# Optimization experiments

Measured on AMD Instinct MI355X. Metric: run time of the kernel, lower is better.

## Reference

```python
import jax, jax.numpy as jnp
import numpy as np

NEG_SLOPE = 0.2  # PyG GATConv default negative_slope
NUM_GRAPHS = 64


def gat_conv(x, src, dst, W, a_src, a_dst, bias, concat):
    """PyG-style GATConv (eval mode, self-loops already appended to src/dst)."""
    N = x.shape[0]
    H, C = a_src.shape
    h = (x @ W).reshape(N, H, C)                      # [N,H,C]
    al_s = jnp.sum(h * a_src, axis=-1)                # [N,H]
    al_d = jnp.sum(h * a_dst, axis=-1)                # [N,H]
    e = jax.nn.leaky_relu(al_s[src] + al_d[dst], NEG_SLOPE)  # [E,H]
    # numerically-stable segment softmax over incoming edges of each dst node
    m = jax.ops.segment_max(e, dst, num_segments=N)   # [N,H]
    ex = jnp.exp(e - m[dst])
    denom = jax.ops.segment_sum(ex, dst, num_segments=N)
    alpha = ex / (denom[dst] + 1e-16)                 # [E,H]
    out = jax.ops.segment_sum(h[src] * alpha[:, :, None], dst, num_segments=N)  # [N,H,C]
    out = out.reshape(N, H * C) if concat else out.mean(axis=1)
    return out + bias


def setup_inputs() -> dict:
    key = jax.random.key(0)
    ks = jax.random.split(key, 32)
    N, E, F_in, H = 20000, 100000, 128, 8
    x = jax.random.normal(ks[0], (N, F_in), jnp.float32)
    edge_index = jax.random.randint(ks[1], (2, E), 0, N, dtype=jnp.int32)
    batch = jnp.sort(jax.random.randint(ks[2], (N,), 0, NUM_GRAPHS, dtype=jnp.int32))
    inp = {"x": x, "edge_index": edge_index, "batch": batch}
    # (fan_in, per-head channels) for conv1..conv_final
    dims = [(F_in, 64), (512, 256), (2048, 256), (2048, 256), (2048, 256)]
    ki = 3
    for i, (fi, c) in enumerate(dims, 1):
        concat = i < 5
        inp[f"W{i}"] = jax.random.normal(ks[ki], (fi, H * c), jnp.float32) * (1.0 / np.sqrt(fi)); ki += 1
        inp[f"a_src{i}"] = jax.random.normal(ks[ki], (H, c), jnp.float32) * 0.1; ki += 1
        inp[f"a_dst{i}"] = jax.random.normal(ks[ki], (H, c), jnp.float32) * 0.1; ki += 1
        inp[f"b{i}"] = jnp.zeros((H * c if concat else c,), jnp.float32)
    inp["W_lin"] = jax.random.normal(ks[ki], (256, 128), jnp.float32) * (1.0 / np.sqrt(256))
    inp["b_lin"] = jnp.zeros((128,), jnp.float32)
    return inp


def reference(x, edge_index, batch,
              W1, a_src1, a_dst1, b1,
              W2, a_src2, a_dst2, b2,
              W3, a_src3, a_dst3, b3,
              W4, a_src4, a_dst4, b4,
              W5, a_src5, a_dst5, b5,
              W_lin, b_lin):
    N = x.shape[0]
    loop = jnp.arange(N, dtype=edge_index.dtype)  # GATConv add_self_loops=True
    src = jnp.concatenate([edge_index[0], loop])
    dst = jnp.concatenate([edge_index[1], loop])
    h = jax.nn.elu(gat_conv(x, src, dst, W1, a_src1, a_dst1, b1, True))
    h = jax.nn.elu(gat_conv(h, src, dst, W2, a_src2, a_dst2, b2, True))
    h = jax.nn.elu(gat_conv(h, src, dst, W3, a_src3, a_dst3, b3, True))
    h = jax.nn.elu(gat_conv(h, src, dst, W4, a_src4, a_dst4, b4, True))
    h = jax.nn.elu(gat_conv(h, src, dst, W5, a_src5, a_dst5, b5, False))
    sums = jax.ops.segment_sum(h, batch, num_segments=NUM_GRAPHS)
    counts = jax.ops.segment_sum(jnp.ones((N, 1), h.dtype), batch, num_segments=NUM_GRAPHS)
    pooled = jax.nn.elu(sums / jnp.maximum(counts, 1.0))  # global_mean_pool + elu
    return pooled @ W_lin + b_lin
```

## Files before the change

### kernel.cpp

```cpp
#include <hip/hip_runtime.h>
#include <hip/hip_fp16.h>
#include <math.h>

#define NHEADS 8
#define NG 64

typedef _Float16 half8_t __attribute__((ext_vector_type(8)));
typedef _Float16 half4_t __attribute__((ext_vector_type(4)));
typedef float    float4_t __attribute__((ext_vector_type(4)));
typedef __attribute__((address_space(1))) const void g_void;
typedef __attribute__((address_space(3))) void l_void;

__device__ __forceinline__ float elu_f(float x)   { return x > 0.f ? x : expf(x) - 1.f; }
__device__ __forceinline__ float lrelu_f(float x) { return x >= 0.f ? x : 0.2f * x; }

__device__ __forceinline__ float4 ld4(const float* p) { return *(const float4*)p; }
__device__ __forceinline__ float4 ld4(const __half* p) {
    const __half2* q = (const __half2*)p;
    __half2 a = q[0], b = q[1];
    return make_float4(__half2float(a.x), __half2float(a.y),
                       __half2float(b.x), __half2float(b.y));
}
__device__ __forceinline__ void st4(float* p, float4 v) { *(float4*)p = v; }
__device__ __forceinline__ void st4(__half* p, float4 v) {
    __half2 a, b;
    a.x = __float2half(v.x); a.y = __float2half(v.y);
    b.x = __float2half(v.z); b.y = __float2half(v.w);
    __half2* q = (__half2*)p; q[0] = a; q[1] = b;
}
__device__ __forceinline__ float scl(float v)  { return v; }
__device__ __forceinline__ float scl(__half v) { return __half2float(v); }
__device__ __forceinline__ void sst(float* p, float v)  { *p = v; }
__device__ __forceinline__ void sst(__half* p, float v) { *p = __float2half(v); }

struct h4s { __half a, b, c, d; };

__global__ void hist_kernel(const int* __restrict__ ei, int E, int Etot, int* __restrict__ counts) {
    int e = blockIdx.x * blockDim.x + threadIdx.x;
    if (e >= Etot) return;
    int dst = (e < E) ? ei[E + e] : (e - E);
    atomicAdd(&counts[dst], 1);
}

__global__ __launch_bounds__(256) void scan_kernel(const int* __restrict__ counts,
                                                   int* __restrict__ offsets,
                                                   int* __restrict__ cursor, int N) {
    __shared__ int wsum[4];
    const int tid = threadIdx.x;
    const int lane = tid & 63, wid = tid >> 6;
    int carry = 0;
    for (int base = 0; base < N; base += 1024) {
        int i0 = base + tid * 4;
        int v0 = 0, v1 = 0, v2 = 0, v3 = 0;
        if (i0 + 3 < N) {
            int4 q = *(const int4*)(counts + i0);
            v0 = q.x; v1 = q.y; v2 = q.z; v3 = q.w;
        } else {
            if (i0     < N) v0 = counts[i0];
            if (i0 + 1 < N) v1 = counts[i0 + 1];
            if (i0 + 2 < N) v2 = counts[i0 + 2];
            if (i0 + 3 < N) v3 = counts[i0 + 3];
        }
        int tsum = v0 + v1 + v2 + v3;
        int incl = tsum;
#pragma unroll
        for (int off = 1; off < 64; off <<= 1) {
            int t = __shfl_up(incl, off);
            if (lane >= off) incl += t;
        }
        if (lane == 63) wsum[wid] = incl;
        __syncthreads();
        int woff = carry;
        for (int w = 0; w < wid; ++w) woff += wsum[w];
        int o0 = woff + incl - tsum;
        int o1 = o0 + v0, o2 = o1 + v1, o3 = o2 + v2;
        if (i0     < N) { offsets[i0]     = o0; cursor[i0]     = o0; }
        if (i0 + 1 < N) { offsets[i0 + 1] = o1; cursor[i0 + 1] = o1; }
        if (i0 + 2 < N) { offsets[i0 + 2] = o2; cursor[i0 + 2] = o2; }
        if (i0 + 3 < N) { offsets[i0 + 3] = o3; cursor[i0 + 3] = o3; }
        __syncthreads();
        carry += wsum[0] + wsum[1] + wsum[2] + wsum[3];
    }
    if (tid == 0) offsets[N] = carry;
}

__global__ void scatter_kernel(const int* __restrict__ ei, int E, int Etot,
                               int* __restrict__ cursor, int* __restrict__ perm_src) {
    int e = blockIdx.x * blockDim.x + threadIdx.x;
    if (e >= Etot) return;
    int src, dst;
    if (e < E) { src = ei[e]; dst = ei[E + e]; }
    else       { src = e - E; dst = e - E; }
    int pos = atomicAdd(&cursor[dst], 1);
    perm_src[pos] = src;
}

struct PrepArgs {
    const float* x; __half* x16; long n4;
    const float* W[5]; __half* T[5];
    int K[5], Nn[5];
    int b0;
    int tb[5];
};

__global__ __launch_bounds__(256) void prep_kernel(PrepArgs a) {
    int bid = blockIdx.x;
    if (bid < a.b0) {
        long i = (long)bid * 256 + threadIdx.x;
        if (i < a.n4) {
            float4 v = ((const float4*)a.x)[i];
            h4s o; o.a = __float2half(v.x); o.b = __float2half(v.y);
            o.c = __float2half(v.z); o.d = __float2half(v.w);
            ((h4s*)a.x16)[i] = o;
        }
        return;
    }
    int l = 0, base = a.b0;
#pragma unroll
    for (int j = 0; j < 4; ++j) if (bid >= a.tb[j]) { l = j + 1; base = a.tb[j]; }
    const float* W = a.W[l]; __half* T = a.T[l];
    int K = a.K[l], Nn = a.Nn[l];
    int t = bid - base;
    int tilesx = Nn >> 5;
    int nb = (t % tilesx) * 32, kb = (t / tilesx) * 32;
    __shared__ float tt[32][33];
    int tx = threadIdx.x & 31, ty = threadIdx.x >> 5;
#pragma unroll
    for (int r = 0; r < 32; r += 8)
        tt[ty + r][tx] = W[(size_t)(kb + ty + r) * Nn + nb + tx];
    __syncthreads();
#pragma unroll
    for (int r = 0; r < 32; r += 8)
        T[(size_t)(nb + ty + r) * K + kb + tx] = __float2half(tt[tx][ty + r]);
}

__global__ __launch_bounds__(256) void gemm_mfma_kernel(const __half* __restrict__ A,
                                                        const __half* __restrict__ Bt,
                                                        __half* __restrict__ C,
                                                        int M, int N, int K) {
    __shared__ __align__(16) __half Asm[128 * 64];
    __shared__ __align__(16) __half Bsm[128 * 64];
    const int tid  = threadIdx.x;
    const int lane = tid & 63;
    const int wave = tid >> 6;

    const int nwg = (int)(gridDim.x * gridDim.y);
    const int lin = (int)(blockIdx.y * gridDim.x + blockIdx.x);
    const int q = nwg >> 3, r = nwg & 7;
    const int xcd = lin & 7, idx = lin >> 3;
    const int nid = (xcd < r ? xcd * (q + 1) : r * (q + 1) + (xcd - r) * q) + idx;
    const int bx = nid % (int)gridDim.x;
    const int by = nid / (int)gridDim.x;
    const int row0 = by * 128;
    const int col0 = bx * 128;

    const int l15 = lane & 15;
    const int l4  = lane >> 4;
    const int wm  = (wave >> 1) * 64;
    const int wn  = (wave & 1) * 64;

    const int sl_row = lane >> 3;
    const int sl_kch = (lane & 7) ^ sl_row;

    float4_t acc[4][4];
#pragma unroll
    for (int i = 0; i < 4; ++i)
#pragma unroll
        for (int j = 0; j < 4; ++j)
            acc[i][j] = (float4_t){0.f, 0.f, 0.f, 0.f};

    for (int k0 = 0; k0 < K; k0 += 64) {
#pragma unroll
        for (int i = 0; i < 4; ++i) {
            int rr = (i * 4 + wave) * 8 + sl_row;
            int ar = row0 + rr; if (ar >= M) ar = M - 1;
            const __half* ga = A + (size_t)ar * K + k0 + sl_kch * 8;
            char* la = (char*)Asm + ((i * 4 + wave) * 1024 + lane * 16);
            __builtin_amdgcn_global_load_lds((g_void*)ga, (l_void*)la, 16, 0, 0);
            const __half* gb = Bt + (size_t)(col0 + rr) * K + k0 + sl_kch * 8;
            char* lb = (char*)Bsm + ((i * 4 + wave) * 1024 + lane * 16);
            __builtin_amdgcn_global_load_lds((g_void*)gb, (l_void*)lb, 16, 0, 0);
        }
        __syncthreads();
#pragma unroll
        for (int kh = 0; kh < 2; ++kh) {
            half8_t af[4], bf[4];
#pragma unroll
            for (int f = 0; f < 4; ++f) {
                int rowa = wm + f * 16 + l15;
                int ca = (kh * 4 + l4) ^ (rowa & 7);
                af[f] = *(const half8_t*)((const char*)Asm + rowa * 128 + ca * 16);
                int rowb = wn + f * 16 + l15;
                int cb = (kh * 4 + l4) ^ (rowb & 7);
                bf[f] = *(const half8_t*)((const char*)Bsm + rowb * 128 + cb * 16);
            }
#pragma unroll
            for (int fm = 0; fm < 4; ++fm)
#pragma unroll
                for (int fn = 0; fn < 4; ++fn)
                    acc[fm][fn] = __builtin_amdgcn_mfma_f32_16x16x32_f16(af[fm], bf[fn], acc[fm][fn], 0, 0, 0);
        }
        __syncthreads();
    }

#pragma unroll
    for (int fm = 0; fm < 4; ++fm) {
#pragma unroll
        for (int r2 = 0; r2 < 4; ++r2) {
            int row = row0 + wm + fm * 16 + l4 * 4 + r2;
            if (row < M) {
#pragma unroll
                for (int fn = 0; fn < 4; ++fn) {
                    int col = col0 + wn + fn * 16 + l15;
                    C[(size_t)row * N + col] = __float2half(acc[fm][fn][r2]);
                }
            }
        }
    }
}

template <typename TA, typename TC>
__global__ __launch_bounds__(256) void gemm_kernel(const TA* __restrict__ A,
                                                   const float* __restrict__ B,
                                                   TC* __restrict__ C,
                                                   int M, int N, int K) {
    __shared__ float As[16][64];
    __shared__ float Bs[16][64];
    const int tid  = threadIdx.x;
    const int row0 = blockIdx.y * 64, col0 = blockIdx.x * 64;
    const int am = tid >> 2, ak = (tid & 3) << 2;
    const int bk = tid >> 4, bn = (tid & 15) << 2;
    const int ty = (tid >> 4) << 2, tx = (tid & 15) << 2;
    float acc[4][4] = {};
    const int arow = row0 + am;
    for (int k0 = 0; k0 < K; k0 += 16) {
        float4 a4 = make_float4(0.f, 0.f, 0.f, 0.f);
        if (arow < M) a4 = ld4(A + (size_t)arow * K + k0 + ak);
        As[ak + 0][am] = a4.x; As[ak + 1][am] = a4.y;
        As[ak + 2][am] = a4.z; As[ak + 3][am] = a4.w;
        *(float4*)&Bs[bk][bn] = *(const float4*)(B + (size_t)(k0 + bk) * N + col0 + bn);
        __syncthreads();
#pragma unroll
        for (int k = 0; k < 16; ++k) {
            float4 ar = *(const float4*)&As[k][ty];
            float4 br = *(const float4*)&Bs[k][tx];
            acc[0][0] += ar.x * br.x; acc[0][1] += ar.x * br.y; acc[0][2] += ar.x * br.z; acc[0][3] += ar.x * br.w;
            acc[1][0] += ar.y * br.x; acc[1][1] += ar.y * br.y; acc[1][2] += ar.y * br.z; acc[1][3] += ar.y * br.w;
            acc[2][0] += ar.z * br.x; acc[2][1] += ar.z * br.y; acc[2][2] += ar.z * br.z; acc[2][3] += ar.z * br.w;
            acc[3][0] += ar.w * br.x; acc[3][1] += ar.w * br.y; acc[3][2] += ar.w * br.z; acc[3][3] += ar.w * br.w;
        }
        __syncthreads();
    }
#pragma unroll
    for (int i = 0; i < 4; ++i) {
        int r = row0 + ty + i;
        if (r < M) {
            float4 o = make_float4(acc[i][0], acc[i][1], acc[i][2], acc[i][3]);
            st4(C + (size_t)r * N + col0 + tx, o);
        }
    }
}

template <int C>
__global__ void al_vec_kernel(const __half* __restrict__ ht, const float* __restrict__ a_src,
                              const float* __restrict__ a_dst, float* __restrict__ al_s,
                              float* __restrict__ al_d, int N) {
    int wid  = (int)((blockIdx.x * blockDim.x + threadIdx.x) >> 6);
    int lane = threadIdx.x & 63;
    if (wid >= N * NHEADS) return;
    int n = wid / NHEADS, h = wid % NHEADS;
    float ss = 0.f, sd = 0.f;
    int c0 = lane * 4;
    if (c0 < C) {
        const __half* hp = ht + (size_t)n * (NHEADS * C) + h * C + c0;
        half4_t v = *(const half4_t*)hp;
        float4 as4 = *(const float4*)(a_src + h * C + c0);
        float4 ad4 = *(const float4*)(a_dst + h * C + c0);
        float v0 = (float)v[0], v1 = (float)v[1], v2 = (float)v[2], v3 = (float)v[3];
        ss = v0 * as4.x + v1 * as4.y + v2 * as4.z + v3 * as4.w;
        sd = v0 * ad4.x + v1 * ad4.y + v2 * ad4.z + v3 * ad4.w;
    }
#pragma unroll
    for (int off = 32; off > 0; off >>= 1) {
        ss += __shfl_down(ss, off);
        sd += __shfl_down(sd, off);
    }
    if (lane == 0) { al_s[wid] = ss; al_d[wid] = sd; }
}

template <int HC, int C, int MODE>
__global__ __launch_bounds__(256) void agg_fused_kernel(const __half* __restrict__ ht,
                                                        const float* __restrict__ al_s,
                                                        const float* __restrict__ al_d,
                                                        const int* __restrict__ offsets,
                                                        const int* __restrict__ perm_src,
                                                        const float* __restrict__ bias,
                                                        void* __restrict__ outv, int N) {
    constexpr int V = HC / 256;
    int n = blockIdx.x;
    int tid = threadIdx.x;
    int lane = tid & 63;
    const int head = (tid * V) / C;
    int s = offsets[n], e = offsets[n + 1];

    int h2 = lane & 7, es = lane >> 3;
    float ad2 = al_d[(size_t)n * 8 + h2];
    float m = -1e30f;
    for (int p0 = s + es; p0 < e; p0 += 8)
        m = fmaxf(m, lrelu_f(al_s[(size_t)perm_src[p0] * 8 + h2] + ad2));
#pragma unroll
    for (int off = 8; off < 64; off <<= 1) m = fmaxf(m, __shfl_xor(m, off));
    float den = 0.f;
    for (int p0 = s + es; p0 < e; p0 += 8)
        den += expf(lrelu_f(al_s[(size_t)perm_src[p0] * 8 + h2] + ad2) - m);
#pragma unroll
    for (int off = 8; off < 64; off <<= 1) den += __shfl_xor(den, off);
    float inv0 = 1.f / (den + 1e-16f);
    float mh   = __shfl(m, head);
    float invh = __shfl(inv0, head);
    float adh  = __shfl(ad2, head);

    float acc[V];
#pragma unroll
    for (int i = 0; i < V; ++i) acc[i] = 0.f;
    const __half* base = ht + (size_t)tid * V;
    int p = s;
    for (; p + 4 <= e; p += 4) {
        int s0 = perm_src[p], s1 = perm_src[p + 1], s2 = perm_src[p + 2], s3 = perm_src[p + 3];
        float a0 = expf(lrelu_f(al_s[(size_t)s0 * 8 + head] + adh) - mh);
        float a1 = expf(lrelu_f(al_s[(size_t)s1 * 8 + head] + adh) - mh);
        float a2 = expf(lrelu_f(al_s[(size_t)s2 * 8 + head] + adh) - mh);
        float a3 = expf(lrelu_f(al_s[(size_t)s3 * 8 + head] + adh) - mh);
        if (V == 8) {
            half8_t v0 = *(const half8_t*)(base + (size_t)s0 * HC);
            half8_t v1 = *(const half8_t*)(base + (size_t)s1 * HC);
            half8_t v2 = *(const half8_t*)(base + (size_t)s2 * HC);
            half8_t v3 = *(const half8_t*)(base + (size_t)s3 * HC);
#pragma unroll
            for (int i = 0; i < 8; ++i) acc[i] += a0 * (float)v0[i];
#pragma unroll
            for (int i = 0; i < 8; ++i) acc[i] += a1 * (float)v1[i];
#pragma unroll
            for (int i = 0; i < 8; ++i) acc[i] += a2 * (float)v2[i];
#pragma unroll
            for (int i = 0; i < 8; ++i) acc[i] += a3 * (float)v3[i];
        } else {
            __half2 w0 = *(const __half2*)(base + (size_t)s0 * HC);
            __half2 w1 = *(const __half2*)(base + (size_t)s1 * HC);
            __half2 w2 = *(const __half2*)(base + (size_t)s2 * HC);
            __half2 w3 = *(const __half2*)(base + (size_t)s3 * HC);
            acc[0] += a0 * __half2float(w0.x); acc[1] += a0 * __half2float(w0.y);
            acc[0] += a1 * __half2float(w1.x); acc[1] += a1 * __half2float(w1.y);
            acc[0] += a2 * __half2float(w2.x); acc[1] += a2 * __half2float(w2.y);
            acc[0] += a3 * __half2float(w3.x); acc[1] += a3 * __half2float(w3.y);
        }
    }
    for (; p < e; ++p) {
        int src = perm_src[p];
        float a = expf(lrelu_f(al_s[(size_t)src * 8 + head] + adh) - mh);
        const __half* hp = base + (size_t)src * HC;
        if (V == 8) {
            half8_t v = *(const half8_t*)hp;
#pragma unroll
            for (int i = 0; i < 8; ++i) acc[i] += a * (float)v[i];
        } else {
            __half2 v2 = *(const __half2*)hp;
            acc[0] += a * __half2float(v2.x);
            acc[1] += a * __half2float(v2.y);
        }
    }
    if (MODE == 0) {
        __half* out = (__half*)outv;
        if (V == 8) {
            half8_t o;
#pragma unroll
            for (int i = 0; i < 8; ++i)
                o[i] = (_Float16)elu_f(acc[i] * invh + bias[tid * 8 + i]);
            *(half8_t*)(out + (size_t)n * HC + tid * 8) = o;
        } else {
            __half2 o;
            o.x = __float2half(elu_f(acc[0] * invh + bias[tid * 2 + 0]));
            o.y = __float2half(elu_f(acc[1] * invh + bias[tid * 2 + 1]));
            *(__half2*)(out + (size_t)n * HC + tid * 2) = o;
        }
    } else {
        __shared__ float sm[256][8];
#pragma unroll
        for (int i = 0; i < 8; ++i) sm[tid][i] = acc[i] * invh;
        __syncthreads();
        float ssum = 0.f;
#pragma unroll
        for (int h = 0; h < 8; ++h) ssum += sm[h * 32 + (tid >> 3)][tid & 7];
        float* out = (float*)outv;
        out[(size_t)n * C + tid] = elu_f(ssum * (1.f / NHEADS) + bias[tid]);
    }
}

template <typename TH>
__global__ void al_kernel(const TH* __restrict__ ht, const float* __restrict__ a_src,
                          const float* __restrict__ a_dst, float* __restrict__ al_s,
                          float* __restrict__ al_d, int N, int C) {
    int wid  = (int)((blockIdx.x * blockDim.x + threadIdx.x) >> 6);
    int lane = threadIdx.x & 63;
    if (wid >= N * NHEADS) return;
    int n = wid / NHEADS, h = wid % NHEADS;
    const TH* hp = ht + (size_t)n * (NHEADS * C) + h * C;
    float ss = 0.f, sd = 0.f;
    for (int c = lane; c < C; c += 64) {
        float v = scl(hp[c]);
        ss += v * a_src[h * C + c];
        sd += v * a_dst[h * C + c];
    }
#pragma unroll
    for (int off = 32; off > 0; off >>= 1) {
        ss += __shfl_down(ss, off);
        sd += __shfl_down(sd, off);
    }
    if (lane == 0) { al_s[wid] = ss; al_d[wid] = sd; }
}

__global__ void alpha_kernel(const int* __restrict__ offsets, const int* __restrict__ perm_src,
                             const float* __restrict__ al_s, const float* __restrict__ al_d,
                             float* __restrict__ alpha, int N) {
    int idx = blockIdx.x * blockDim.x + threadIdx.x;
    if (idx >= N * NHEADS) return;
    int n = idx / NHEADS, h = idx % NHEADS;
    int s = offsets[n], e = offsets[n + 1];
    float ad = al_d[idx];
    float m = -1e30f;
    for (int p = s; p < e; ++p) {
        float v = lrelu_f(al_s[perm_src[p] * NHEADS + h] + ad);
        m = fmaxf(m, v);
    }
    float denom = 0.f;
    for (int p = s; p < e; ++p) {
        float v  = lrelu_f(al_s[perm_src[p] * NHEADS + h] + ad);
        float ex = expf(v - m);
        alpha[(size_t)p * NHEADS + h] = ex;
        denom += ex;
    }
    float inv = 1.f / (denom + 1e-16f);
    for (int p = s; p < e; ++p) alpha[(size_t)p * NHEADS + h] *= inv;
}

template <int HC, int C, int MODE, typename TH, typename TO>
__global__ __launch_bounds__(256) void agg_kernel(const TH* __restrict__ ht,
                                                  const float* __restrict__ alpha,
                                                  const int* __restrict__ offsets,
                                                  const int* __restrict__ perm_src,
                                                  const float* __restrict__ bias,
                                                  TO* __restrict__ out, int N) {
    constexpr int PER = HC / 256;
    int n = blockIdx.x;
    int tid = threadIdx.x;
    float acc[PER];
#pragma unroll
    for (int i = 0; i < PER; ++i) acc[i] = 0.f;
    int s = offsets[n], e = offsets[n + 1];
    for (int p = s; p < e; ++p) {
        int src = perm_src[p];
        const TH* hp = ht + (size_t)src * HC;
#pragma unroll
        for (int i = 0; i < PER; ++i) {
            int j = tid + i * 256;
            float a = alpha[(size_t)p * NHEADS + (j / C)];
            acc[i] += a * scl(hp[j]);
        }
    }
    if (MODE == 0) {
#pragma unroll
        for (int i = 0; i < PER; ++i) {
            int j = tid + i * 256;
            sst(&out[(size_t)n * HC + j], elu_f(acc[i] + bias[j]));
        }
    } else {
        float srow = 0.f;
#pragma unroll
        for (int i = 0; i < PER; ++i) srow += acc[i];
        sst(&out[(size_t)n * C + tid], elu_f(srow * (1.f / NHEADS) + bias[tid]));
    }
}

__global__ void gstart_kernel(const int* __restrict__ batch, int* __restrict__ gstart, int N) {
    int n = blockIdx.x * blockDim.x + threadIdx.x;
    if (n > N) return;
    if (n == 0) {
        int b0 = batch[0];
        for (int g = 0; g <= b0; ++g) gstart[g] = 0;
    } else if (n == N) {
        int bl = batch[N - 1];
        for (int g = bl + 1; g <= NG; ++g) gstart[g] = N;
    } else {
        int bp = batch[n - 1], bc = batch[n];
        for (int g = bp + 1; g <= bc; ++g) gstart[g] = n;
    }
}

__global__ void pool_kernel(const float* __restrict__ h5, const int* __restrict__ gstart,
                            float* __restrict__ pooled) {
    int g = blockIdx.x, c = threadIdx.x;
    int s = gstart[g], e = gstart[g + 1];
    float sum = 0.f;
    for (int n = s; n < e; ++n) sum += h5[(size_t)n * 256 + c];
    float cnt = fmaxf((float)(e - s), 1.f);
    pooled[g * 256 + c] = elu_f(sum / cnt);
}

__global__ void linear_kernel(const float* __restrict__ pooled, const float* __restrict__ W,
                              const float* __restrict__ b, float* __restrict__ out) {
    int g = blockIdx.x, c = threadIdx.x;
    float s = b[c];
    for (int k = 0; k < 256; ++k) s += pooled[g * 256 + k] * W[k * 128 + c];
    out[g * 128 + c] = s;
}

__device__ __forceinline__ int lb_dev(const int* a, int n, int key) {
    int lo = 0, hi = n;
    while (lo < hi) { int mid = (lo + hi) >> 1; if (a[mid] < key) lo = mid + 1; else hi = mid; }
    return lo;
}

__global__ __launch_bounds__(256) void pool_linear_kernel(const float* __restrict__ h5,
                                                          const int* __restrict__ batch, int N,
                                                          const float* __restrict__ Wlin,
                                                          const float* __restrict__ blin,
                                                          float* __restrict__ out) {
    int g = blockIdx.x, c = threadIdx.x;
    int s = lb_dev(batch, N, g);
    int e = lb_dev(batch, N, g + 1);
    __shared__ float pooled_s[256];
    float sum = 0.f;
    for (int n = s; n < e; ++n) sum += h5[(size_t)n * 256 + c];
    float cnt = fmaxf((float)(e - s), 1.f);
    pooled_s[c] = elu_f(sum / cnt);
    __syncthreads();
    if (c < 128) {
        float acc = blin[c];
        for (int k = 0; k < 256; ++k) acc += pooled_s[k] * Wlin[k * 128 + c];
        out[g * 128 + c] = acc;
    }
}

template <typename TIO, typename TH>
static void run_pipeline(const float* x, const float* const* W, const float* const* asrc,
                         const float* const* adst, const float* const* bias,
                         char* rawIO, char* rawHT,
                         float* al_s, float* al_d, float* alpha_buf,
                         const int* offsets, const int* perm_src,
                         int N, hipStream_t stream) {
    TIO* bufIO = (TIO*)rawIO;
    TH*  bufHT = (TH*)rawHT;
    {
        dim3 g(512 / 64, (N + 63) / 64);
        gemm_kernel<float, TH><<<g, 256, 0, stream>>>(x, W[0], bufHT, N, 512, 128);
        al_kernel<TH><<<(N * NHEADS * 64 + 255) / 256, 256, 0, stream>>>(bufHT, asrc[0], adst[0], al_s, al_d, N, 64);
        alpha_kernel<<<(N * NHEADS + 255) / 256, 256, 0, stream>>>(offsets, perm_src, al_s, al_d, alpha_buf, N);
        agg_kernel<512, 64, 0, TH, TIO><<<N, 256, 0, stream>>>(bufHT, alpha_buf, offsets, perm_src, bias[0], bufIO, N);
    }
    int Kdim = 512;
    for (int l = 1; l < 5; ++l) {
        dim3 g(2048 / 64, (N + 63) / 64);
        gemm_kernel<TIO, TH><<<g, 256, 0, stream>>>(bufIO, W[l], bufHT, N, 2048, Kdim);
        al_kernel<TH><<<(N * NHEADS * 64 + 255) / 256, 256, 0, stream>>>(bufHT, asrc[l], adst[l], al_s, al_d, N, 256);
        alpha_kernel<<<(N * NHEADS + 255) / 256, 256, 0, stream>>>(offsets, perm_src, al_s, al_d, alpha_buf, N);
        if (l < 4)
            agg_kernel<2048, 256, 0, TH, TIO><<<N, 256, 0, stream>>>(bufHT, alpha_buf, offsets, perm_src, bias[l], bufIO, N);
        else
            agg_kernel<2048, 256, 1, TH, float><<<N, 256, 0, stream>>>(bufHT, alpha_buf, offsets, perm_src, bias[l], (float*)rawIO, N);
        Kdim = 2048;
    }
}

extern "C" void kernel_launch(void* const* d_in, const int* in_sizes, int n_in,
                              void* d_out, int out_size, void* d_ws, size_t ws_size,
                              hipStream_t stream) {
    const float* x     = (const float*)d_in[0];
    const int*   ei    = (const int*)d_in[1];
    const int*   batch = (const int*)d_in[2];
    const float* W[5]    = {(const float*)d_in[3],  (const float*)d_in[7],  (const float*)d_in[11],
                            (const float*)d_in[15], (const float*)d_in[19]};
    const float* asrc[5] = {(const float*)d_in[4],  (const float*)d_in[8],  (const float*)d_in[12],
                            (const float*)d_in[16], (const float*)d_in[20]};
    const float* adst[5] = {(const float*)d_in[5],  (const float*)d_in[9],  (const float*)d_in[13],
                            (const float*)d_in[17], (const float*)d_in[21]};
    const float* bias[5] = {(const float*)d_in[6],  (const float*)d_in[10], (const float*)d_in[14],
                            (const float*)d_in[18], (const float*)d_in[22]};
    const float* Wlin = (const float*)d_in[23];
    const float* blin = (const float*)d_in[24];

    const int N    = in_sizes[0] / 128;
    const int E    = in_sizes[1] / 2;
    const int Etot = E + N;

    auto align256 = [](size_t b) { return (b + 255) & ~(size_t)255; };

    size_t sz_counts = align256((size_t)N * 4);
    size_t sz_off    = align256((size_t)(N + 1) * 4);
    size_t sz_cur    = align256((size_t)N * 4);
    size_t sz_perm   = align256((size_t)Etot * 4);
    size_t sz_al     = align256((size_t)N * NHEADS * 4);
    size_t sz_alpha  = align256((size_t)Etot * NHEADS * 4);
    size_t sz_gst    = align256((size_t)(NG + 1) * 4);
    size_t sz_pool   = align256((size_t)NG * 256 * 4);
    size_t misc = sz_counts + sz_off + sz_cur + sz_perm + 2 * sz_al + sz_alpha + sz_gst + sz_pool;

    size_t bigf  = align256((size_t)N * 2048 * sizeof(float));
    size_t bigh  = align256((size_t)N * 2048 * sizeof(__half));
    const int Kd[5] = {128, 512, 2048, 2048, 2048};
    const int Nd[5] = {512, 2048, 2048, 2048, 2048};
    size_t sz_wt_each[5], sz_wt_all = 0;
    for (int l = 0; l < 5; ++l) { sz_wt_each[l] = align256((size_t)Kd[l] * Nd[l] * sizeof(__half)); sz_wt_all += sz_wt_each[l]; }
    size_t sz_x16 = align256((size_t)N * 128 * sizeof(__half));

    int path;
    if      (ws_size >= misc + 2 * bigh + sz_wt_all + sz_x16) path = 3;
    else if (ws_size >= misc + 2 * bigf)                      path = 0;
    else if (ws_size >= misc + bigf + bigh)                   path = 1;
    else if (ws_size >= misc + 2 * bigh)                      path = 2;
    else {
        hipMemsetAsync(d_out, 0, (size_t)out_size * sizeof(float), stream);
        return;
    }

    char* ws = (char*)d_ws;
    size_t off = 0;
    auto carve = [&](size_t bytes) { void* p = ws + off; off += bytes; return p; };
    int*   counts   = (int*)carve(sz_counts);
    int*   offsets  = (int*)carve(sz_off);
    int*   cursor   = (int*)carve(sz_cur);
    int*   perm_src = (int*)carve(sz_perm);
    float* al_s     = (float*)carve(sz_al);
    float* al_d     = (float*)carve(sz_al);
    float* alpha    = (float*)carve(sz_alpha);
    int*   gstart   = (int*)carve(sz_gst);
    float* pooled   = (float*)carve(sz_pool);

    hipMemsetAsync(counts, 0, (size_t)N * 4, stream);
    hist_kernel<<<(Etot + 255) / 256, 256, 0, stream>>>(ei, E, Etot, counts);
    scan_kernel<<<1, 256, 0, stream>>>(counts, offsets, cursor, N);
    scatter_kernel<<<(Etot + 255) / 256, 256, 0, stream>>>(ei, E, Etot, cursor, perm_src);

    if (path == 3) {
        char*   rawIO = (char*)carve(bigh);
        char*   rawHT = (char*)carve(bigh);
        __half* Wt[5];
        for (int l = 0; l < 5; ++l) Wt[l] = (__half*)carve(sz_wt_each[l]);
        __half* x16   = (__half*)carve(sz_x16);
        __half* bufIO = (__half*)rawIO;
        __half* bufHT = (__half*)rawHT;

        PrepArgs pa;
        pa.x = x; pa.x16 = x16; pa.n4 = (long)N * 128 / 4;
        for (int l = 0; l < 5; ++l) { pa.W[l] = W[l]; pa.T[l] = Wt[l]; pa.K[l] = Kd[l]; pa.Nn[l] = Nd[l]; }
        int bacc = (int)((pa.n4 + 255) / 256);
        pa.b0 = bacc;
        for (int l = 0; l < 5; ++l) { bacc += (Nd[l] / 32) * (Kd[l] / 32); pa.tb[l] = bacc; }
        prep_kernel<<<bacc, 256, 0, stream>>>(pa);

        const __half* curA = x16;
        int Kdim = 128;
        for (int l = 0; l < 5; ++l) {
            const int C  = (l == 0) ? 64 : 256;
            const int HC = NHEADS * C;
            {
                dim3 gg(HC / 128, (N + 127) / 128);
                gemm_mfma_kernel<<<gg, 256, 0, stream>>>(curA, Wt[l], bufHT, N, HC, Kdim);
            }
            if (l == 0)
                al_vec_kernel<64><<<(N * NHEADS * 64 + 255) / 256, 256, 0, stream>>>(bufHT, asrc[l], adst[l], al_s, al_d, N);
            else
                al_vec_kernel<256><<<(N * NHEADS * 64 + 255) / 256, 256, 0, stream>>>(bufHT, asrc[l], adst[l], al_s, al_d, N);
            if (l == 0)
                agg_fused_kernel<512, 64, 0><<<N, 256, 0, stream>>>(bufHT, al_s, al_d, offsets, perm_src, bias[l], bufIO, N);
            else if (l < 4)
                agg_fused_kernel<2048, 256, 0><<<N, 256, 0, stream>>>(bufHT, al_s, al_d, offsets, perm_src, bias[l], bufIO, N);
            else
                agg_fused_kernel<2048, 256, 1><<<N, 256, 0, stream>>>(bufHT, al_s, al_d, offsets, perm_src, bias[l], (float*)rawIO, N);
            curA = bufIO;
            Kdim = (l == 0) ? 512 : 2048;
        }
        pool_linear_kernel<<<NG, 256, 0, stream>>>((const float*)rawIO, batch, N, Wlin, blin, (float*)d_out);
        return;
    }

    char* rawIO = (char*)carve(path == 2 ? bigh : bigf);
    char* rawHT = (char*)carve(path == 0 ? bigf : bigh);

    if (path == 0)
        run_pipeline<float, float>(x, W, asrc, adst, bias, rawIO, rawHT, al_s, al_d, alpha, offsets, perm_src, N, stream);
    else if (path == 1)
        run_pipeline<float, __half>(x, W, asrc, adst, bias, rawIO, rawHT, al_s, al_d, alpha, offsets, perm_src, N, stream);
    else
        run_pipeline<__half, __half>(x, W, asrc, adst, bias, rawIO, rawHT, al_s, al_d, alpha, offsets, perm_src, N, stream);

    gstart_kernel<<<(N + 1 + 255) / 256, 256, 0, stream>>>(batch, gstart, N);
    pool_kernel<<<NG, 256, 0, stream>>>((const float*)rawIO, gstart, pooled);
    linear_kernel<<<NG, 128, 0, stream>>>(pooled, Wlin, blin, (float*)d_out);
}
```

Before: 1.261 ms.

## Replace 128x128 MFMA GEMM with 256x256 double-buffered, phase-pipelined kernel

Swaps the single-buffered 128x128 tile fp16 MFMA GEMM for a 512-thread 256x256 tile kernel. It double-buffers LDS and splits each k-step into four quadrant phases, interleaving global-to-LDS loads for the next tile with MFMA work, using partial vmcnt waits and s_setprio around the MFMA bursts. Larger tiles cut global traffic per flop and the pipelining hides load latency. The cost is more registers and LDS (128KB per block), fewer blocks for the small layer-1 GEMM, and fragile hand-tuned wait counts.

```diff
diff --git a/kernel.cpp b/kernel.cpp
--- a/kernel.cpp
+++ b/kernel.cpp
@@ -134,15 +134,28 @@
         T[(size_t)(nb + ty + r) * K + kb + tx] = __float2half(tt[tx][ty + r]);
 }
 
-__global__ __launch_bounds__(256) void gemm_mfma_kernel(const __half* __restrict__ A,
-                                                        const __half* __restrict__ Bt,
-                                                        __half* __restrict__ C,
-                                                        int M, int N, int K) {
-    __shared__ __align__(16) __half Asm[128 * 64];
-    __shared__ __align__(16) __half Bsm[128 * 64];
+#define MMA_PHASE(MH, NH)                                                      \
+  __builtin_amdgcn_s_setprio(1);                                               \
+  { _Pragma("unroll") for (int f_ = 0; f_ < 4; ++f_) {                         \
+      _Pragma("unroll") for (int g_ = 0; g_ < 2; ++g_) {                       \
+        _Pragma("unroll") for (int kk_ = 0; kk_ < 2; ++kk_)                    \
+          acc[(MH) * 2 + (NH)][f_][g_] =                                       \
+              __builtin_amdgcn_mfma_f32_16x16x32_f16(                          \
+                  af[f_][kk_], bf[g_][kk_],                                    \
+                  acc[(MH) * 2 + (NH)][f_][g_], 0, 0, 0);                      \
+  } } }                                                                        \
+  __builtin_amdgcn_s_setprio(0);
+
+__global__ __launch_bounds__(512, 2) void gemm_mfma256_kernel(const __half* __restrict__ A,
+                                                              const __half* __restrict__ Bt,
+                                                              __half* __restrict__ C,
+                                                              int M, int N, int K) {
+    __shared__ __half lds[2][2][16384];
     const int tid  = threadIdx.x;
     const int lane = tid & 63;
     const int wave = tid >> 6;
+    const int wr   = wave >> 2;
+    const int wc   = wave & 3;
 
     const int nwg = (int)(gridDim.x * gridDim.y);
     const int lin = (int)(blockIdx.y * gridDim.x + blockIdx.x);
@@ -151,68 +164,120 @@
     const int nid = (xcd < r ? xcd * (q + 1) : r * (q + 1) + (xcd - r) * q) + idx;
     const int bx = nid % (int)gridDim.x;
     const int by = nid / (int)gridDim.x;
-    const int row0 = by * 128;
-    const int col0 = bx * 128;
-
-    const int l15 = lane & 15;
-    const int l4  = lane >> 4;
-    const int wm  = (wave >> 1) * 64;
-    const int wn  = (wave & 1) * 64;
-
-    const int sl_row = lane >> 3;
-    const int sl_kch = (lane & 7) ^ sl_row;
-
-    float4_t acc[4][4];
+    const int row0 = by * 256;
+    const int col0 = bx * 256;
+
+    const int l15 = lane & 15, l4 = lane >> 4;
+    const int srow = tid >> 3;
+    const int kch  = (tid & 7) ^ (srow & 7);
+
+    float4_t acc[4][4][2];
 #pragma unroll
     for (int i = 0; i < 4; ++i)
 #pragma unroll
         for (int j = 0; j < 4; ++j)
-            acc[i][j] = (float4_t){0.f, 0.f, 0.f, 0.f};
-
-    for (int k0 = 0; k0 < K; k0 += 64) {
-#pragma unroll
-        for (int i = 0; i < 4; ++i) {
-            int rr = (i * 4 + wave) * 8 + sl_row;
-            int ar = row0 + rr; if (ar >= M) ar = M - 1;
-            const __half* ga = A + (size_t)ar * K + k0 + sl_kch * 8;
-            char* la = (char*)Asm + ((i * 4 + wave) * 1024 + lane * 16);
-            __builtin_amdgcn_global_load_lds((g_void*)ga, (l_void*)la, 16, 0, 0);
-            const __half* gb = Bt + (size_t)(col0 + rr) * K + k0 + sl_kch * 8;
-            char* lb = (char*)Bsm + ((i * 4 + wave) * 1024 + lane * 16);
-            __builtin_amdgcn_global_load_lds((g_void*)gb, (l_void*)lb, 16, 0, 0);
-        }
-        __syncthreads();
-#pragma unroll
-        for (int kh = 0; kh < 2; ++kh) {
-            half8_t af[4], bf[4];
-#pragma unroll
-            for (int f = 0; f < 4; ++f) {
-                int rowa = wm + f * 16 + l15;
-                int ca = (kh * 4 + l4) ^ (rowa & 7);
-                af[f] = *(const half8_t*)((const char*)Asm + rowa * 128 + ca * 16);
-                int rowb = wn + f * 16 + l15;
-                int cb = (kh * 4 + l4) ^ (rowb & 7);
-                bf[f] = *(const half8_t*)((const char*)Bsm + rowb * 128 + cb * 16);
+#pragma unroll
+            for (int g = 0; g < 2; ++g)
+                acc[i][j][g] = (float4_t){0.f, 0.f, 0.f, 0.f};
+
+    auto stageA = [&](int cb, int kt, int halfsel) {
+#pragma unroll
+        for (int sub = 0; sub < 2; ++sub) {
+            int rr = halfsel * 128 + sub * 64 + srow;
+            int gr = row0 + rr; if (gr >= M) gr = M - 1;
+            const __half* g = A + (size_t)gr * K + kt * 64 + kch * 8;
+            __half* l = &lds[cb][0][(halfsel * 128 + sub * 64) * 64] + tid * 8;
+            __builtin_amdgcn_global_load_lds((g_void*)g, (l_void*)l, 16, 0, 0);
+        }
+    };
+    auto stageB = [&](int cb, int kt, int halfsel) {
+#pragma unroll
+        for (int sub = 0; sub < 2; ++sub) {
+            int rr = halfsel * 128 + sub * 64 + srow;
+            const __half* g = Bt + (size_t)(col0 + rr) * K + kt * 64 + kch * 8;
+            __half* l = &lds[cb][1][(halfsel * 128 + sub * 64) * 64] + tid * 8;
+            __builtin_amdgcn_global_load_lds((g_void*)g, (l_void*)l, 16, 0, 0);
+        }
+    };
+
+    half8_t af[4][2], bf[2][2];
+    auto ldA = [&](int cb, int mh) {
+        const char* base = (const char*)&lds[cb][0][0];
+#pragma unroll
+        for (int f = 0; f < 4; ++f) {
+            int row = mh * 128 + wr * 64 + f * 16 + l15;
+#pragma unroll
+            for (int kk = 0; kk < 2; ++kk) {
+                int ch = (kk * 4 + l4) ^ (row & 7);
+                af[f][kk] = *(const half8_t*)(base + row * 128 + ch * 16);
             }
-#pragma unroll
-            for (int fm = 0; fm < 4; ++fm)
-#pragma unroll
-                for (int fn = 0; fn < 4; ++fn)
-                    acc[fm][fn] = __builtin_amdgcn_mfma_f32_16x16x32_f16(af[fm], bf[fn], acc[fm][fn], 0, 0, 0);
-        }
-        __syncthreads();
-    }
-
-#pragma unroll
-    for (int fm = 0; fm < 4; ++fm) {
-#pragma unroll
-        for (int r2 = 0; r2 < 4; ++r2) {
-            int row = row0 + wm + fm * 16 + l4 * 4 + r2;
-            if (row < M) {
-#pragma unroll
-                for (int fn = 0; fn < 4; ++fn) {
-                    int col = col0 + wn + fn * 16 + l15;
-                    C[(size_t)row * N + col] = __float2half(acc[fm][fn][r2]);
+        }
+    };
+    auto ldB = [&](int cb, int nh) {
+        const char* base = (const char*)&lds[cb][1][0];
+#pragma unroll
+        for (int f = 0; f < 2; ++f) {
+            int row = nh * 128 + wc * 32 + f * 16 + l15;
+#pragma unroll
+            for (int kk = 0; kk < 2; ++kk) {
+                int ch = (kk * 4 + l4) ^ (row & 7);
+                bf[f][kk] = *(const half8_t*)(base + row * 128 + ch * 16);
+            }
+        }
+    };
+
+    const int nt = K >> 6;
+    stageA(0, 0, 0); stageB(0, 0, 0); stageB(0, 0, 1); stageA(0, 0, 1);
+
+    for (int t = 0; t < nt; ++t) {
+        int cb = t & 1, nb = cb ^ 1;
+        int ktn = (t + 1 < nt) ? t + 1 : t;
+
+        stageA(nb, ktn, 0);
+        __builtin_amdgcn_sched_barrier(0);
+        asm volatile("s_waitcnt vmcnt(6)" ::: "memory");
+        __builtin_amdgcn_s_barrier();
+        __builtin_amdgcn_sched_barrier(0);
+        ldA(cb, 0); ldB(cb, 0);
+        MMA_PHASE(0, 0)
+
+        stageB(nb, ktn, 0);
+        __builtin_amdgcn_sched_barrier(0);
+        asm volatile("s_waitcnt vmcnt(6)" ::: "memory");
+        __builtin_amdgcn_s_barrier();
+        __builtin_amdgcn_sched_barrier(0);
+        ldB(cb, 1);
+        MMA_PHASE(0, 1)
+
+        stageB(nb, ktn, 1);
+        __builtin_amdgcn_sched_barrier(0);
+        asm volatile("s_waitcnt vmcnt(6)" ::: "memory");
+        __builtin_amdgcn_s_barrier();
+        __builtin_amdgcn_sched_barrier(0);
+        ldA(cb, 1);
+        MMA_PHASE(1, 1)
+
+        stageA(nb, ktn, 1);
+        ldB(cb, 0);
+        MMA_PHASE(1, 0)
+    }
+
+#pragma unroll
+    for (int mh = 0; mh < 2; ++mh) {
+#pragma unroll
+        for (int nh = 0; nh < 2; ++nh) {
+#pragma unroll
+            for (int fm = 0; fm < 4; ++fm) {
+#pragma unroll
+                for (int r2 = 0; r2 < 4; ++r2) {
+                    int row = row0 + mh * 128 + wr * 64 + fm * 16 + l4 * 4 + r2;
+                    if (row < M) {
+#pragma unroll
+                        for (int fn = 0; fn < 2; ++fn) {
+                            int col = col0 + nh * 128 + wc * 32 + fn * 16 + l15;
+                            C[(size_t)row * N + col] = __float2half(acc[mh * 2 + nh][fm][fn][r2]);
+                        }
+                    }
                 }
             }
         }
@@ -663,8 +728,8 @@
             const int C  = (l == 0) ? 64 : 256;
             const int HC = NHEADS * C;
             {
-                dim3 gg(HC / 128, (N + 127) / 128);
-                gemm_mfma_kernel<<<gg, 256, 0, stream>>>(curA, Wt[l], bufHT, N, HC, Kdim);
+                dim3 gg(HC / 256, (N + 255) / 256);
+                gemm_mfma256_kernel<<<gg, 512, 0, stream>>>(curA, Wt[l], bufHT, N, HC, Kdim);
             }
             if (l == 0)
                 al_vec_kernel<64><<<(N * NHEADS * 64 + 255) / 256, 256, 0, stream>>>(bufHT, asrc[l], adst[l], al_s, al_d, N);
```

Result: faster. 1.192 ms (-5.5%).
